# Kernel tuning notes

Measured on AMD Instinct MI355X. Metric: run time of the kernel, lower is better.

## Reference

```python
import jax, jax.numpy as jnp
import numpy as np

NUM_CLUSTERS = 32
EPS = 1e-12

def _l2norm(v, axis):
    return v / jnp.maximum(jnp.linalg.norm(v, axis=axis, keepdims=True), EPS)

def setup_inputs() -> dict:
    key = jax.random.key(0)
    k1, k2, k3 = jax.random.split(key, 3)
    B, M, D, K = 64, 512, 2048, NUM_CLUSTERS
    init_sc = 1.0 / np.sqrt(D)
    x = jax.random.normal(k1, (B, M, D), dtype=jnp.float32)
    W = init_sc * jax.random.normal(k2, (K, D), dtype=jnp.float32)
    centroids = init_sc * jax.random.normal(k3, (K, D), dtype=jnp.float32)
    return {"x": x, "W": W, "centroids": centroids}

def reference(x, W, centroids):
    # x: [B, M, D] frame features; W: [K, D]; centroids: [K, D]
    xn = _l2norm(x, axis=-1)                              # per-frame L2 normalize
    sa = jax.nn.softmax(jnp.einsum('bmd,kd->bmk', xn, W), axis=-1)  # [B, M, K]
    # vlad[b,k,d] = sum_m sa[b,m,k] * (xn[b,m,d] - centroids[k,d])
    #            = (sa^T @ xn)[b,k,d] - colsum(sa)[b,k] * centroids[k,d]
    agg = jnp.einsum('bmk,bmd->bkd', sa, xn)              # [B, K, D]
    vlad = agg - jnp.sum(sa, axis=1)[..., None] * centroids[None]
    vlad = _l2norm(vlad, axis=2)                          # intra-normalize per cluster
    vlad = vlad.reshape(vlad.shape[0], -1)                # [B, K*D]
    return _l2norm(vlad, axis=1)
```

## Files before the change

### kernel.cpp

```cpp
#include <hip/hip_runtime.h>
#include <hip/hip_bf16.h>
#include <cstdint>
#include <cstddef>

#define Bn 64
#define Mn 512
#define Dn 2048
#define Kn 32
#define EPSF 1e-12f

typedef __attribute__((ext_vector_type(8))) __bf16 bf16x8;
typedef __attribute__((ext_vector_type(4))) __bf16 bf16x4;
typedef __attribute__((ext_vector_type(4))) float f32x4;

__global__ __launch_bounds__(256) void k1_logits_softmax(const float* __restrict__ x,
                                                         const float* __restrict__ W,
                                                         __bf16* __restrict__ saT,
                                                         float* __restrict__ colsum) {
  int wv = threadIdx.x >> 6, lane = threadIdx.x & 63;
  int mr = lane & 15, q = lane >> 4;
  int blk = 511 - blockIdx.x;
  int row0 = (blk * 4 + wv) * 16;
  int b = row0 >> 9;
  const float* xp = x + (size_t)(row0 + mr) * Dn + q * 8;
  const float* wp0 = W + (size_t)mr * Dn + q * 8;
  const float* wp1 = W + (size_t)(mr + 16) * Dn + q * 8;
  f32x4 acc0 = {0.f, 0.f, 0.f, 0.f};
  f32x4 acc1 = {0.f, 0.f, 0.f, 0.f};
  float ssq = 0.f;
#pragma unroll 2
  for (int s = 0; s < 64; ++s) {
    f32x4 xa = *(const f32x4*)(xp + s * 32);
    f32x4 xb = *(const f32x4*)(xp + s * 32 + 4);
    bf16x8 af;
    af[0] = (__bf16)xa[0]; af[1] = (__bf16)xa[1];
    af[2] = (__bf16)xa[2]; af[3] = (__bf16)xa[3];
    af[4] = (__bf16)xb[0]; af[5] = (__bf16)xb[1];
    af[6] = (__bf16)xb[2]; af[7] = (__bf16)xb[3];
    ssq = fmaf(xa[0], xa[0], ssq); ssq = fmaf(xa[1], xa[1], ssq);
    ssq = fmaf(xa[2], xa[2], ssq); ssq = fmaf(xa[3], xa[3], ssq);
    ssq = fmaf(xb[0], xb[0], ssq); ssq = fmaf(xb[1], xb[1], ssq);
    ssq = fmaf(xb[2], xb[2], ssq); ssq = fmaf(xb[3], xb[3], ssq);
    f32x4 wa = *(const f32x4*)(wp0 + s * 32);
    f32x4 wb = *(const f32x4*)(wp0 + s * 32 + 4);
    bf16x8 b0;
    b0[0] = (__bf16)wa[0]; b0[1] = (__bf16)wa[1];
    b0[2] = (__bf16)wa[2]; b0[3] = (__bf16)wa[3];
    b0[4] = (__bf16)wb[0]; b0[5] = (__bf16)wb[1];
    b0[6] = (__bf16)wb[2]; b0[7] = (__bf16)wb[3];
    f32x4 wc = *(const f32x4*)(wp1 + s * 32);
    f32x4 wd = *(const f32x4*)(wp1 + s * 32 + 4);
    bf16x8 b1;
    b1[0] = (__bf16)wc[0]; b1[1] = (__bf16)wc[1];
    b1[2] = (__bf16)wc[2]; b1[3] = (__bf16)wc[3];
    b1[4] = (__bf16)wd[0]; b1[5] = (__bf16)wd[1];
    b1[6] = (__bf16)wd[2]; b1[7] = (__bf16)wd[3];
    acc0 = __builtin_amdgcn_mfma_f32_16x16x32_bf16(af, b0, acc0, 0, 0, 0);
    acc1 = __builtin_amdgcn_mfma_f32_16x16x32_bf16(af, b1, acc1, 0, 0, 0);
  }
  ssq += __shfl_xor(ssq, 16);
  ssq += __shfl_xor(ssq, 32);
  float invb = 1.f / fmaxf(sqrtf(ssq), EPSF);
  float cs0 = 0.f, cs1 = 0.f;
  bf16x4 v40, v41;
#pragma unroll
  for (int r = 0; r < 4; ++r) {
    float inv = __shfl(invb, q * 4 + r);
    float v0 = acc0[r] * inv, v1 = acc1[r] * inv;
    float mx = fmaxf(v0, v1);
    mx = fmaxf(mx, __shfl_xor(mx, 1));
    mx = fmaxf(mx, __shfl_xor(mx, 2));
    mx = fmaxf(mx, __shfl_xor(mx, 4));
    mx = fmaxf(mx, __shfl_xor(mx, 8));
    float e0 = __expf(v0 - mx), e1 = __expf(v1 - mx);
    float sm = e0 + e1;
    sm += __shfl_xor(sm, 1); sm += __shfl_xor(sm, 2);
    sm += __shfl_xor(sm, 4); sm += __shfl_xor(sm, 8);
    float rs = 1.f / sm;
    float sa0 = e0 * rs, sa1 = e1 * rs;
    v40[r] = (__bf16)(sa0 * inv);
    v41[r] = (__bf16)(sa1 * inv);
    cs0 += sa0; cs1 += sa1;
  }
  int mloc = row0 & 511;
  __bf16* st = saT + ((size_t)(b * Kn + mr)) * Mn + mloc + q * 4;
  *(bf16x4*)st = v40;
  *(bf16x4*)(st + (size_t)16 * Mn) = v41;
  cs0 += __shfl_xor(cs0, 16); cs0 += __shfl_xor(cs0, 32);
  cs1 += __shfl_xor(cs1, 16); cs1 += __shfl_xor(cs1, 32);
  if (lane < 16) {
    atomicAdd(&colsum[b * Kn + mr], cs0);
    atomicAdd(&colsum[b * Kn + mr + 16], cs1);
  }
}

#define AS 520
__global__ __launch_bounds__(256) void k3_agg(const float* __restrict__ x,
                                              const __bf16* __restrict__ saT,
                                              const float* __restrict__ colsum,
                                              const float* __restrict__ cent,
                                              float* __restrict__ vlad,
                                              float* __restrict__ ssq) {
  __shared__ __bf16 sal[Kn * AS];
  __shared__ float csl[Kn];
  int b = blockIdx.x >> 4;
  int dchunk = (blockIdx.x & 15) * 128;
  int t = threadIdx.x;
  const __bf16* sg = saT + (size_t)b * Kn * Mn;
#pragma unroll
  for (int i = 0; i < 8; ++i) {
    int u = t + 256 * i;
    int kr = u >> 6, off = (u & 63) * 8;
    *(bf16x8*)&sal[kr * AS + off] = *(const bf16x8*)(sg + (size_t)kr * Mn + off);
  }
  if (t < Kn) csl[t] = colsum[b * Kn + t];
  __syncthreads();
  int w = t >> 6, lane = t & 63;
  int n = lane & 15, q = lane >> 4;
  int d0 = dchunk + w * 32;
  const float* xg = x + (size_t)b * Mn * Dn;
  f32x4 acc[2][2] = {};
  for (int m0 = 0; m0 < Mn; m0 += 32) {
    bf16x8 a0 = *(const bf16x8*)&sal[n * AS + m0 + q * 8];
    bf16x8 a1 = *(const bf16x8*)&sal[(n + 16) * AS + m0 + q * 8];
#pragma unroll
    for (int dt = 0; dt < 2; ++dt) {
      const float* xp = xg + (size_t)(m0 + q * 8) * Dn + d0 + dt * 16 + n;
      bf16x8 bv;
#pragma unroll
      for (int j = 0; j < 8; ++j) bv[j] = (__bf16)xp[(size_t)j * Dn];
      acc[dt][0] = __builtin_amdgcn_mfma_f32_16x16x32_bf16(a0, bv, acc[dt][0], 0, 0, 0);
      acc[dt][1] = __builtin_amdgcn_mfma_f32_16x16x32_bf16(a1, bv, acc[dt][1], 0, 0, 0);
    }
  }
#pragma unroll
  for (int dt = 0; dt < 2; ++dt) {
#pragma unroll
    for (int kt = 0; kt < 2; ++kt) {
#pragma unroll
      for (int r = 0; r < 4; ++r) {
        int k = kt * 16 + q * 4 + r;
        int d = d0 + dt * 16 + n;
        float vv = acc[dt][kt][r] - csl[k] * cent[(size_t)k * Dn + d];
        vlad[((size_t)(b * Kn + k)) * Dn + d] = vv;
        float sq = vv * vv;
        sq += __shfl_xor(sq, 1); sq += __shfl_xor(sq, 2);
        sq += __shfl_xor(sq, 4); sq += __shfl_xor(sq, 8);
        if (n == 0) atomicAdd(&ssq[b * Kn + k], sq);
      }
    }
  }
}

__global__ __launch_bounds__(256) void k4_norm(float* __restrict__ out,
                                               const float* __restrict__ ssq) {
  __shared__ float rk[Kn];
  __shared__ float us[Kn];
  int b = blockIdx.x >> 4;
  int t = threadIdx.x;
  if (t < Kn) {
    float ss = ssq[b * Kn + t];
    float r = 1.f / fmaxf(sqrtf(ss), EPSF);
    rk[t] = r;
    us[t] = ss * r * r;
  }
  __syncthreads();
  float S = 0.f;
#pragma unroll
  for (int k = 0; k < Kn; ++k) S += us[k];
  float s = 1.f / fmaxf(sqrtf(S), EPSF);
  int chunk = blockIdx.x & 15;
  size_t base = (size_t)b * (Kn * Dn) + (size_t)chunk * 4096;
  f32x4* p = (f32x4*)(out + base);
#pragma unroll
  for (int i = 0; i < 4; ++i) {
    int idx = t + 256 * i;
    int k = (chunk * 4096 + idx * 4) >> 11;
    f32x4 v = p[idx];
    float sc = rk[k] * s;
    v[0] *= sc; v[1] *= sc; v[2] *= sc; v[3] *= sc;
    p[idx] = v;
  }
}

extern "C" void kernel_launch(void* const* d_in, const int* in_sizes, int n_in,
                              void* d_out, int out_size, void* d_ws, size_t ws_size,
                              hipStream_t stream) {
  const float* x = (const float*)d_in[0];
  const float* W = (const float*)d_in[1];
  const float* cent = (const float*)d_in[2];
  float* out = (float*)d_out;
  char* ws = (char*)d_ws;
  float* colsum = (float*)ws;
  float* ssqb = (float*)(ws + 8192);
  __bf16* saT = (__bf16*)(ws + 16384);
  hipMemsetAsync(ws, 0, 16384, stream);
  hipLaunchKernelGGL(k1_logits_softmax, dim3(512), dim3(256), 0, stream, x, W, saT, colsum);
  hipLaunchKernelGGL(k3_agg, dim3(1024), dim3(256), 0, stream, x, saT, colsum, cent, out, ssqb);
  hipLaunchKernelGGL(k4_norm, dim3(1024), dim3(256), 0, stream, out, ssqb);
}
```

Baseline: 441.9 us.

## Cache bf16 x copy in logits kernel, pre-convert W, retile aggregation kernel

Pre-converts W to bf16 once, and splits the logits kernel's D reduction across two wave pairs combined through LDS. When workspace allows, it also writes a bf16 copy of x. The aggregation kernel reads that half-width copy instead of fp32 x and uses smaller d-chunks with double-buffered saT tiles in LDS instead of staging the whole saT matrix. The intent is to cut k3 memory traffic and LDS footprint to raise occupancy, at the cost of extra bf16 writes in k1 and a large workspace requirement.

```diff
diff --git a/kernel.cpp b/kernel.cpp
--- a/kernel.cpp
+++ b/kernel.cpp
@@ -13,51 +13,64 @@
 typedef __attribute__((ext_vector_type(4))) __bf16 bf16x4;
 typedef __attribute__((ext_vector_type(4))) float f32x4;
 
-__global__ __launch_bounds__(256) void k1_logits_softmax(const float* __restrict__ x,
-                                                         const float* __restrict__ W,
-                                                         __bf16* __restrict__ saT,
-                                                         float* __restrict__ colsum) {
+__global__ __launch_bounds__(256) void k0_wcvt(const float* __restrict__ W,
+                                               __bf16* __restrict__ wbf) {
+  int i = (blockIdx.x * 256 + threadIdx.x) * 4;
+  f32x4 v = *(const f32x4*)(W + i);
+  bf16x4 o;
+  o[0] = (__bf16)v[0]; o[1] = (__bf16)v[1]; o[2] = (__bf16)v[2]; o[3] = (__bf16)v[3];
+  *(bf16x4*)(wbf + i) = o;
+}
+
+template <bool XBF>
+__global__ __launch_bounds__(256, 4) void k1_logits_softmax(const float* __restrict__ x,
+                                                            const __bf16* __restrict__ Wb,
+                                                            __bf16* __restrict__ saT,
+                                                            float* __restrict__ colsum,
+                                                            __bf16* __restrict__ xbf) {
+  __shared__ float red[2][64][9];
   int wv = threadIdx.x >> 6, lane = threadIdx.x & 63;
+  int g = wv & 1, h = wv >> 1;
   int mr = lane & 15, q = lane >> 4;
-  int blk = 511 - blockIdx.x;
-  int row0 = (blk * 4 + wv) * 16;
-  int b = row0 >> 9;
-  const float* xp = x + (size_t)(row0 + mr) * Dn + q * 8;
-  const float* wp0 = W + (size_t)mr * Dn + q * 8;
-  const float* wp1 = W + (size_t)(mr + 16) * Dn + q * 8;
+  int blk = blockIdx.x;
+  int row0 = blk * 32 + g * 16;
+  int b = blk >> 4;
+  const float* xp = x + (size_t)(row0 + mr) * Dn + h * 1024 + q * 8;
+  const __bf16* wp0 = Wb + (size_t)mr * Dn + h * 1024 + q * 8;
+  const __bf16* wp1 = Wb + (size_t)(mr + 16) * Dn + h * 1024 + q * 8;
+  __bf16* xs = XBF ? (xbf + (size_t)(row0 + mr) * Dn + h * 1024 + q * 8) : nullptr;
   f32x4 acc0 = {0.f, 0.f, 0.f, 0.f};
   f32x4 acc1 = {0.f, 0.f, 0.f, 0.f};
   float ssq = 0.f;
 #pragma unroll 2
-  for (int s = 0; s < 64; ++s) {
+  for (int s = 0; s < 32; ++s) {
     f32x4 xa = *(const f32x4*)(xp + s * 32);
     f32x4 xb = *(const f32x4*)(xp + s * 32 + 4);
+    bf16x8 b0 = *(const bf16x8*)(wp0 + s * 32);
+    bf16x8 b1 = *(const bf16x8*)(wp1 + s * 32);
     bf16x8 af;
     af[0] = (__bf16)xa[0]; af[1] = (__bf16)xa[1];
     af[2] = (__bf16)xa[2]; af[3] = (__bf16)xa[3];
     af[4] = (__bf16)xb[0]; af[5] = (__bf16)xb[1];
     af[6] = (__bf16)xb[2]; af[7] = (__bf16)xb[3];
+    if constexpr (XBF) *(bf16x8*)(xs + s * 32) = af;
     ssq = fmaf(xa[0], xa[0], ssq); ssq = fmaf(xa[1], xa[1], ssq);
     ssq = fmaf(xa[2], xa[2], ssq); ssq = fmaf(xa[3], xa[3], ssq);
     ssq = fmaf(xb[0], xb[0], ssq); ssq = fmaf(xb[1], xb[1], ssq);
     ssq = fmaf(xb[2], xb[2], ssq); ssq = fmaf(xb[3], xb[3], ssq);
-    f32x4 wa = *(const f32x4*)(wp0 + s * 32);
-    f32x4 wb = *(const f32x4*)(wp0 + s * 32 + 4);
-    bf16x8 b0;
-    b0[0] = (__bf16)wa[0]; b0[1] = (__bf16)wa[1];
-    b0[2] = (__bf16)wa[2]; b0[3] = (__bf16)wa[3];
-    b0[4] = (__bf16)wb[0]; b0[5] = (__bf16)wb[1];
-    b0[6] = (__bf16)wb[2]; b0[7] = (__bf16)wb[3];
-    f32x4 wc = *(const f32x4*)(wp1 + s * 32);
-    f32x4 wd = *(const f32x4*)(wp1 + s * 32 + 4);
-    bf16x8 b1;
-    b1[0] = (__bf16)wc[0]; b1[1] = (__bf16)wc[1];
-    b1[2] = (__bf16)wc[2]; b1[3] = (__bf16)wc[3];
-    b1[4] = (__bf16)wd[0]; b1[5] = (__bf16)wd[1];
-    b1[6] = (__bf16)wd[2]; b1[7] = (__bf16)wd[3];
     acc0 = __builtin_amdgcn_mfma_f32_16x16x32_bf16(af, b0, acc0, 0, 0, 0);
     acc1 = __builtin_amdgcn_mfma_f32_16x16x32_bf16(af, b1, acc1, 0, 0, 0);
   }
+  if (h == 1) {
+#pragma unroll
+    for (int r = 0; r < 4; ++r) { red[g][lane][r] = acc0[r]; red[g][lane][4 + r] = acc1[r]; }
+    red[g][lane][8] = ssq;
+  }
+  __syncthreads();
+  if (h == 1) return;
+#pragma unroll
+  for (int r = 0; r < 4; ++r) { acc0[r] += red[g][lane][r]; acc1[r] += red[g][lane][4 + r]; }
+  ssq += red[g][lane][8];
   ssq += __shfl_xor(ssq, 16);
   ssq += __shfl_xor(ssq, 32);
   float invb = 1.f / fmaxf(sqrtf(ssq), EPSF);
@@ -94,60 +107,63 @@
   }
 }
 
-#define AS 520
-__global__ __launch_bounds__(256) void k3_agg(const float* __restrict__ x,
-                                              const __bf16* __restrict__ saT,
-                                              const float* __restrict__ colsum,
-                                              const float* __restrict__ cent,
-                                              float* __restrict__ vlad,
-                                              float* __restrict__ ssq) {
-  __shared__ __bf16 sal[Kn * AS];
+template <bool XBF>
+__global__ __launch_bounds__(256, 6) void k3_agg(const float* __restrict__ x,
+                                                 const __bf16* __restrict__ xbf,
+                                                 const __bf16* __restrict__ saT,
+                                                 const float* __restrict__ colsum,
+                                                 const float* __restrict__ cent,
+                                                 float* __restrict__ vlad,
+                                                 float* __restrict__ ssq) {
+  __shared__ __bf16 tile[2][Kn][40];
   __shared__ float csl[Kn];
-  int b = blockIdx.x >> 4;
-  int dchunk = (blockIdx.x & 15) * 128;
+  int b = blockIdx.x >> 5;
+  int chunk = blockIdx.x & 31;
   int t = threadIdx.x;
-  const __bf16* sg = saT + (size_t)b * Kn * Mn;
-#pragma unroll
-  for (int i = 0; i < 8; ++i) {
-    int u = t + 256 * i;
-    int kr = u >> 6, off = (u & 63) * 8;
-    *(bf16x8*)&sal[kr * AS + off] = *(const bf16x8*)(sg + (size_t)kr * Mn + off);
-  }
-  if (t < Kn) csl[t] = colsum[b * Kn + t];
-  __syncthreads();
   int w = t >> 6, lane = t & 63;
   int n = lane & 15, q = lane >> 4;
-  int d0 = dchunk + w * 32;
-  const float* xg = x + (size_t)b * Mn * Dn;
-  f32x4 acc[2][2] = {};
-  for (int m0 = 0; m0 < Mn; m0 += 32) {
-    bf16x8 a0 = *(const bf16x8*)&sal[n * AS + m0 + q * 8];
-    bf16x8 a1 = *(const bf16x8*)&sal[(n + 16) * AS + m0 + q * 8];
-#pragma unroll
-    for (int dt = 0; dt < 2; ++dt) {
-      const float* xp = xg + (size_t)(m0 + q * 8) * Dn + d0 + dt * 16 + n;
-      bf16x8 bv;
+  int d0 = chunk * 64 + w * 16;
+  int sk = t >> 3, mo = (t & 7) * 4;
+  const __bf16* sg = saT + ((size_t)b * Kn + sk) * Mn + mo;
+  if (t < Kn) csl[t] = colsum[b * Kn + t];
+  *(bf16x4*)&tile[0][sk][mo] = *(const bf16x4*)sg;
+  const float* xgf = x + (size_t)b * Mn * Dn + d0 + n;
+  const __bf16* xgb = XBF ? (xbf + (size_t)b * Mn * Dn + d0 + n) : nullptr;
+  f32x4 acc[2] = {};
+  for (int it = 0; it < 16; ++it) {
+    int m0 = it * 32;
+    int cb = it & 1;
+    __syncthreads();
+    bf16x4 stg = {};
+    if (it < 15) stg = *(const bf16x4*)(sg + m0 + 32);
+    bf16x8 bv;
+    if constexpr (XBF) {
+      const __bf16* xp = xgb + (size_t)(m0 + q * 8) * Dn;
+#pragma unroll
+      for (int j = 0; j < 8; ++j) bv[j] = xp[(size_t)j * Dn];
+    } else {
+      const float* xp = xgf + (size_t)(m0 + q * 8) * Dn;
 #pragma unroll
       for (int j = 0; j < 8; ++j) bv[j] = (__bf16)xp[(size_t)j * Dn];
-      acc[dt][0] = __builtin_amdgcn_mfma_f32_16x16x32_bf16(a0, bv, acc[dt][0], 0, 0, 0);
-      acc[dt][1] = __builtin_amdgcn_mfma_f32_16x16x32_bf16(a1, bv, acc[dt][1], 0, 0, 0);
     }
-  }
-#pragma unroll
-  for (int dt = 0; dt < 2; ++dt) {
-#pragma unroll
-    for (int kt = 0; kt < 2; ++kt) {
-#pragma unroll
-      for (int r = 0; r < 4; ++r) {
-        int k = kt * 16 + q * 4 + r;
-        int d = d0 + dt * 16 + n;
-        float vv = acc[dt][kt][r] - csl[k] * cent[(size_t)k * Dn + d];
-        vlad[((size_t)(b * Kn + k)) * Dn + d] = vv;
-        float sq = vv * vv;
-        sq += __shfl_xor(sq, 1); sq += __shfl_xor(sq, 2);
-        sq += __shfl_xor(sq, 4); sq += __shfl_xor(sq, 8);
-        if (n == 0) atomicAdd(&ssq[b * Kn + k], sq);
-      }
+    bf16x8 a0 = *(const bf16x8*)&tile[cb][n][q * 8];
+    bf16x8 a1 = *(const bf16x8*)&tile[cb][n + 16][q * 8];
+    acc[0] = __builtin_amdgcn_mfma_f32_16x16x32_bf16(a0, bv, acc[0], 0, 0, 0);
+    acc[1] = __builtin_amdgcn_mfma_f32_16x16x32_bf16(a1, bv, acc[1], 0, 0, 0);
+    if (it < 15) *(bf16x4*)&tile[cb ^ 1][sk][mo] = stg;
+  }
+  const float* cg = cent + d0 + n;
+#pragma unroll
+  for (int kt = 0; kt < 2; ++kt) {
+#pragma unroll
+    for (int r = 0; r < 4; ++r) {
+      int k = kt * 16 + q * 4 + r;
+      float vv = acc[kt][r] - csl[k] * cg[(size_t)k * Dn];
+      vlad[((size_t)(b * Kn + k)) * Dn + d0 + n] = vv;
+      float sq = vv * vv;
+      sq += __shfl_xor(sq, 1); sq += __shfl_xor(sq, 2);
+      sq += __shfl_xor(sq, 4); sq += __shfl_xor(sq, 8);
+      if (n == 0) atomicAdd(&ssq[b * Kn + k], sq);
     }
   }
 }
@@ -193,9 +209,19 @@
   char* ws = (char*)d_ws;
   float* colsum = (float*)ws;
   float* ssqb = (float*)(ws + 8192);
-  __bf16* saT = (__bf16*)(ws + 16384);
+  __bf16* wbf = (__bf16*)(ws + 16384);
+  __bf16* saT = (__bf16*)(ws + 16384 + 131072);
+  __bf16* xbf = (__bf16*)(ws + 16384 + 131072 + 2097152);
+  size_t need_xbf = 16384 + 131072 + 2097152 + (size_t)Bn * Mn * Dn * 2;
+  bool use_xbf = ws_size >= need_xbf;
   hipMemsetAsync(ws, 0, 16384, stream);
-  hipLaunchKernelGGL(k1_logits_softmax, dim3(512), dim3(256), 0, stream, x, W, saT, colsum);
-  hipLaunchKernelGGL(k3_agg, dim3(1024), dim3(256), 0, stream, x, saT, colsum, cent, out, ssqb);
-  hipLaunchKernelGGL(k4_norm, dim3(1024), dim3(256), 0, stream, out, ssqb);
-}
+  k0_wcvt<<<dim3(64), dim3(256), 0, stream>>>(W, wbf);
+  if (use_xbf) {
+    k1_logits_softmax<true><<<dim3(1024), dim3(256), 0, stream>>>(x, wbf, saT, colsum, xbf);
+    k3_agg<true><<<dim3(2048), dim3(256), 0, stream>>>(x, xbf, saT, colsum, cent, out, ssqb);
+  } else {
+    k1_logits_softmax<false><<<dim3(1024), dim3(256), 0, stream>>>(x, wbf, saT, colsum, nullptr);
+    k3_agg<false><<<dim3(2048), dim3(256), 0, stream>>>(x, nullptr, saT, colsum, cent, out, ssqb);
+  }
+  k4_norm<<<dim3(1024), dim3(256), 0, stream>>>(out, ssqb);
+}
```

New measurement: 446.6 us. Within noise of the previous version (+1.1%).

## Stage x rows in swizzled LDS, split K across waves, pre-convert W to bf16

Applied to the files above, without the earlier changes.

A new tiny kernel converts W to bf16 once per call. The logits kernel now gives each block 16 rows, not 64. It loads them coalesced into XOR-swizzled shared memory as bf16 while computing row norms, then splits the D reduction across four waves and combines the partial MFMA accumulators through LDS. This is meant to fix the old strided per-lane x loads and the repeated fp32 W conversion. The cost is an extra launch, 64KB of LDS per block, and more barriers, with three of the four waves idle during the softmax.

```diff
diff --git a/kernel.cpp b/kernel.cpp
--- a/kernel.cpp
+++ b/kernel.cpp
@@ -13,59 +13,93 @@
 typedef __attribute__((ext_vector_type(4))) __bf16 bf16x4;
 typedef __attribute__((ext_vector_type(4))) float f32x4;
 
-__global__ __launch_bounds__(256) void k1_logits_softmax(const float* __restrict__ x,
-                                                         const float* __restrict__ W,
-                                                         __bf16* __restrict__ saT,
-                                                         float* __restrict__ colsum) {
+__global__ __launch_bounds__(256) void k0_wcvt(const float* __restrict__ W,
+                                               __bf16* __restrict__ wbf) {
+  int i = (blockIdx.x * 256 + threadIdx.x) * 4;
+  f32x4 v = *(const f32x4*)(W + i);
+  bf16x4 o;
+  o[0] = (__bf16)v[0]; o[1] = (__bf16)v[1]; o[2] = (__bf16)v[2]; o[3] = (__bf16)v[3];
+  *(bf16x4*)(wbf + i) = o;
+}
+
+__global__ __launch_bounds__(256, 2) void k1_logits_softmax(const float* __restrict__ x,
+                                                            const __bf16* __restrict__ Wb,
+                                                            __bf16* __restrict__ saT,
+                                                            float* __restrict__ colsum) {
+  __shared__ char salb[16 * 4096];
   int wv = threadIdx.x >> 6, lane = threadIdx.x & 63;
+  int h = wv;
   int mr = lane & 15, q = lane >> 4;
-  int blk = 511 - blockIdx.x;
-  int row0 = (blk * 4 + wv) * 16;
-  int b = row0 >> 9;
-  const float* xp = x + (size_t)(row0 + mr) * Dn + q * 8;
-  const float* wp0 = W + (size_t)mr * Dn + q * 8;
-  const float* wp1 = W + (size_t)(mr + 16) * Dn + q * 8;
+  int blk = 2047 - blockIdx.x;
+  int row0 = blk * 16;
+  int b = blk >> 5;
+  const float* xr = x + ((size_t)row0 + h * 4) * Dn + lane * 4;
+  float rs0, rs1, rs2, rs3;
+#pragma unroll
+  for (int r4 = 0; r4 < 4; ++r4) {
+    const float* rp = xr + (size_t)r4 * Dn;
+    int lrow = h * 4 + r4;
+    int rbase = lrow << 12;
+    int rxor = (lrow & 7) << 4;
+    float sq = 0.f;
+#pragma unroll
+    for (int i = 0; i < 8; ++i) {
+      f32x4 v = *(const f32x4*)(rp + i * 256);
+      bf16x4 o;
+      o[0] = (__bf16)v[0]; o[1] = (__bf16)v[1];
+      o[2] = (__bf16)v[2]; o[3] = (__bf16)v[3];
+      sq = fmaf(v[0], v[0], sq); sq = fmaf(v[1], v[1], sq);
+      sq = fmaf(v[2], v[2], sq); sq = fmaf(v[3], v[3], sq);
+      *(bf16x4*)(salb + rbase + ((i * 512 + lane * 8) ^ rxor)) = o;
+    }
+    sq += __shfl_xor(sq, 1); sq += __shfl_xor(sq, 2); sq += __shfl_xor(sq, 4);
+    sq += __shfl_xor(sq, 8); sq += __shfl_xor(sq, 16); sq += __shfl_xor(sq, 32);
+    if (r4 == 0) rs0 = sq; else if (r4 == 1) rs1 = sq;
+    else if (r4 == 2) rs2 = sq; else rs3 = sq;
+  }
+  __syncthreads();
+  const __bf16* wp0 = Wb + (size_t)mr * Dn + h * 512 + q * 8;
+  const __bf16* wp1 = wp0 + (size_t)16 * Dn;
+  int rbase = mr << 12;
+  int rxor = (mr & 7) << 4;
+  int cbase = h * 1024 + q * 16;
   f32x4 acc0 = {0.f, 0.f, 0.f, 0.f};
   f32x4 acc1 = {0.f, 0.f, 0.f, 0.f};
-  float ssq = 0.f;
-#pragma unroll 2
-  for (int s = 0; s < 64; ++s) {
-    f32x4 xa = *(const f32x4*)(xp + s * 32);
-    f32x4 xb = *(const f32x4*)(xp + s * 32 + 4);
-    bf16x8 af;
-    af[0] = (__bf16)xa[0]; af[1] = (__bf16)xa[1];
-    af[2] = (__bf16)xa[2]; af[3] = (__bf16)xa[3];
-    af[4] = (__bf16)xb[0]; af[5] = (__bf16)xb[1];
-    af[6] = (__bf16)xb[2]; af[7] = (__bf16)xb[3];
-    ssq = fmaf(xa[0], xa[0], ssq); ssq = fmaf(xa[1], xa[1], ssq);
-    ssq = fmaf(xa[2], xa[2], ssq); ssq = fmaf(xa[3], xa[3], ssq);
-    ssq = fmaf(xb[0], xb[0], ssq); ssq = fmaf(xb[1], xb[1], ssq);
-    ssq = fmaf(xb[2], xb[2], ssq); ssq = fmaf(xb[3], xb[3], ssq);
-    f32x4 wa = *(const f32x4*)(wp0 + s * 32);
-    f32x4 wb = *(const f32x4*)(wp0 + s * 32 + 4);
-    bf16x8 b0;
-    b0[0] = (__bf16)wa[0]; b0[1] = (__bf16)wa[1];
-    b0[2] = (__bf16)wa[2]; b0[3] = (__bf16)wa[3];
-    b0[4] = (__bf16)wb[0]; b0[5] = (__bf16)wb[1];
-    b0[6] = (__bf16)wb[2]; b0[7] = (__bf16)wb[3];
-    f32x4 wc = *(const f32x4*)(wp1 + s * 32);
-    f32x4 wd = *(const f32x4*)(wp1 + s * 32 + 4);
-    bf16x8 b1;
-    b1[0] = (__bf16)wc[0]; b1[1] = (__bf16)wc[1];
-    b1[2] = (__bf16)wc[2]; b1[3] = (__bf16)wc[3];
-    b1[4] = (__bf16)wd[0]; b1[5] = (__bf16)wd[1];
-    b1[6] = (__bf16)wd[2]; b1[7] = (__bf16)wd[3];
+#pragma unroll 4
+  for (int ks = 0; ks < 16; ++ks) {
+    bf16x8 af = *(const bf16x8*)(salb + rbase + ((cbase + ks * 64) ^ rxor));
+    bf16x8 b0 = *(const bf16x8*)(wp0 + ks * 32);
+    bf16x8 b1 = *(const bf16x8*)(wp1 + ks * 32);
     acc0 = __builtin_amdgcn_mfma_f32_16x16x32_bf16(af, b0, acc0, 0, 0, 0);
     acc1 = __builtin_amdgcn_mfma_f32_16x16x32_bf16(af, b1, acc1, 0, 0, 0);
   }
-  ssq += __shfl_xor(ssq, 16);
-  ssq += __shfl_xor(ssq, 32);
-  float invb = 1.f / fmaxf(sqrtf(ssq), EPSF);
+  __syncthreads();
+  float* redf = (float*)salb;
+  if (h) {
+    float* rp2 = redf + ((h - 1) * 64 + lane) * 8;
+#pragma unroll
+    for (int r = 0; r < 4; ++r) { rp2[r] = acc0[r]; rp2[4 + r] = acc1[r]; }
+  }
+  if (lane == 0) {
+    float* spw = redf + 1536 + h * 4;
+    spw[0] = rs0; spw[1] = rs1; spw[2] = rs2; spw[3] = rs3;
+  }
+  __syncthreads();
+  if (h) return;
+#pragma unroll
+  for (int r = 0; r < 4; ++r) {
+    acc0[r] += redf[(0 * 64 + lane) * 8 + r] + redf[(1 * 64 + lane) * 8 + r]
+             + redf[(2 * 64 + lane) * 8 + r];
+    acc1[r] += redf[(0 * 64 + lane) * 8 + 4 + r] + redf[(1 * 64 + lane) * 8 + 4 + r]
+             + redf[(2 * 64 + lane) * 8 + 4 + r];
+  }
+  const float* sp = redf + 1536;
   float cs0 = 0.f, cs1 = 0.f;
   bf16x4 v40, v41;
 #pragma unroll
   for (int r = 0; r < 4; ++r) {
-    float inv = __shfl(invb, q * 4 + r);
+    float ssr = sp[q * 4 + r];
+    float inv = 1.f / fmaxf(sqrtf(ssr), EPSF);
     float v0 = acc0[r] * inv, v1 = acc1[r] * inv;
     float mx = fmaxf(v0, v1);
     mx = fmaxf(mx, __shfl_xor(mx, 1));
@@ -76,8 +110,8 @@
     float sm = e0 + e1;
     sm += __shfl_xor(sm, 1); sm += __shfl_xor(sm, 2);
     sm += __shfl_xor(sm, 4); sm += __shfl_xor(sm, 8);
-    float rs = 1.f / sm;
-    float sa0 = e0 * rs, sa1 = e1 * rs;
+    float rsi = 1.f / sm;
+    float sa0 = e0 * rsi, sa1 = e1 * rsi;
     v40[r] = (__bf16)(sa0 * inv);
     v41[r] = (__bf16)(sa1 * inv);
     cs0 += sa0; cs1 += sa1;
@@ -193,9 +227,11 @@
   char* ws = (char*)d_ws;
   float* colsum = (float*)ws;
   float* ssqb = (float*)(ws + 8192);
-  __bf16* saT = (__bf16*)(ws + 16384);
+  __bf16* wbf = (__bf16*)(ws + 16384);
+  __bf16* saT = (__bf16*)(ws + 16384 + 131072);
   hipMemsetAsync(ws, 0, 16384, stream);
-  hipLaunchKernelGGL(k1_logits_softmax, dim3(512), dim3(256), 0, stream, x, W, saT, colsum);
-  hipLaunchKernelGGL(k3_agg, dim3(1024), dim3(256), 0, stream, x, saT, colsum, cent, out, ssqb);
-  hipLaunchKernelGGL(k4_norm, dim3(1024), dim3(256), 0, stream, out, ssqb);
-}
+  k0_wcvt<<<dim3(64), dim3(256), 0, stream>>>(W, wbf);
+  k1_logits_softmax<<<dim3(2048), dim3(256), 0, stream>>>(x, wbf, saT, colsum);
+  k3_agg<<<dim3(1024), dim3(256), 0, stream>>>(x, saT, colsum, cent, out, ssqb);
+  k4_norm<<<dim3(1024), dim3(256), 0, stream>>>(out, ssqb);
+}
```

Result: no change. 443.3 us (+0.3%).
